# Performance work log

Measured on AMD Instinct MI355X. Metric: run time of the kernel, lower is better.

Reference implementation:

```python
import jax, jax.numpy as jnp
import numpy as np

# Dims: B batch, C=P channels (features per pixel), H*W=N pixels, M ELM models, Q=1 hidden units
M, Q, B, C, H, W_SP = 4, 1, 32, 1024, 28, 28
P = C
N = H * W_SP
EPS = 1e-10


def _lcg_weights(m, n, seed):
    """Deterministic LCG pseudo-random weights, z-score standardized (ELM_AE init)."""
    L = m * n
    a, b, c = L + 2, L + 3, float(L) ** 2
    v = np.zeros(L, dtype=np.float64)
    v[0] = seed + 1.0
    for i in range(1, L):
        v[i] = (a * v[i - 1] + b) % c
    v = (v - v.mean()) / (v.std() + EPS)
    return v.reshape(m, n).astype(np.float32)


def setup_inputs() -> dict:
    key = jax.random.key(0)
    x = jax.random.normal(key, (B, C, H, W_SP), dtype=jnp.float32)
    # One Q x P random input-weight matrix per ELM model, seed = model * (Q * P)
    Wm = jnp.stack([jnp.asarray(_lcg_weights(Q, P, model * (Q * P))) for model in range(M)])  # [M, Q, P]
    return {"x": x, "Wm": Wm}


def reference(x, Wm):
    b, c, h, w = x.shape
    # _norm('l2', ...): per-channel L2 normalization over (h, w), as F.normalize(dim=(1,2))
    norms = jnp.linalg.norm(x.reshape(b, c, h * w), axis=-1)[:, :, None, None]  # [B, C, 1, 1]
    xn = x / jnp.maximum(norms, EPS)
    X = xn.reshape(b, c, h * w)  # meta activation map per sample: [B, P, N]
    # ELM-AE hidden layer, batched over (sample, model): g = sigmoid(W @ X)
    G = jax.nn.sigmoid(jnp.einsum('mqp,bpn->bmqn', Wm, X))  # [B, M, Q, N]
    # fit_AE: output weights beta = pinv(g^T) @ X^T  -> [Q, P]
    pinvGt = jnp.linalg.pinv(jnp.swapaxes(G, -1, -2))       # [B, M, Q, N]
    beta = jnp.einsum('bmqn,bpn->bmqp', pinvGt, X)          # [B, M, Q, P]
    # sum over the M models; Q == 1 so flatten (Q, P) -> Q*P features
    feats = beta.sum(axis=1).reshape(b, -1)                 # [B, Q*P]
    return jnp.nan_to_num(feats)
```

## Files before the change

### kernel.cpp

```cpp
#include <hip/hip_runtime.h>
#include <math.h>

#define BATCH 32
#define CH    1024
#define NPix  784
#define MMOD  4
#define NPC   64
#define PPC   16
#define K1B   256
#define NF4   196
#define T2    832

__device__ __forceinline__ float wave_reduce(float s) {
    #pragma unroll
    for (int off = 32; off; off >>= 1) s += __shfl_down(s, off, 64);
    return s;
}

__device__ __forceinline__ float dpp_wave_sum(float v) {
    int x;
    x = __builtin_amdgcn_update_dpp(0, __builtin_bit_cast(int, v), 0x111, 0xf, 0xf, true);
    v += __builtin_bit_cast(float, x);
    x = __builtin_amdgcn_update_dpp(0, __builtin_bit_cast(int, v), 0x112, 0xf, 0xf, true);
    v += __builtin_bit_cast(float, x);
    x = __builtin_amdgcn_update_dpp(0, __builtin_bit_cast(int, v), 0x114, 0xf, 0xf, true);
    v += __builtin_bit_cast(float, x);
    x = __builtin_amdgcn_update_dpp(0, __builtin_bit_cast(int, v), 0x118, 0xf, 0xf, true);
    v += __builtin_bit_cast(float, x);
    x = __builtin_amdgcn_update_dpp(0, __builtin_bit_cast(int, v), 0x142, 0xa, 0xf, true);
    v += __builtin_bit_cast(float, x);
    x = __builtin_amdgcn_update_dpp(0, __builtin_bit_cast(int, v), 0x143, 0xc, 0xf, true);
    v += __builtin_bit_cast(float, x);
    return v;
}

__global__ __launch_bounds__(K1B) void k_nz(const float* __restrict__ x,
                                            const float* __restrict__ Wm,
                                            float* __restrict__ inv_norm,
                                            float* __restrict__ zpart) {
    __shared__ float sq_l[PPC][4];
    __shared__ float4 wl4[PPC];
    const int blk = blockIdx.x;
    const int b  = blk >> 6;
    const int pc = blk & (NPC - 1);
    const int t = threadIdx.x;
    const int wv = t >> 6, lane = t & 63;
    const bool act = (t < NF4);
    const float4* xb4 = (const float4*)(x + ((size_t)b * CH + (size_t)pc * PPC) * NPix);
    const int tt = act ? t : 0;

    float4 xv[PPC];
    #pragma unroll
    for (int pp = 0; pp < PPC; pp++) xv[pp] = xb4[pp * NF4 + tt];

    #pragma unroll
    for (int pp = 0; pp < PPC; pp++) {
        float4 v = xv[pp];
        float s = act ? (v.x*v.x + v.y*v.y + v.z*v.z + v.w*v.w) : 0.f;
        s = dpp_wave_sum(s);
        if (lane == 63) sq_l[pp][wv] = s;
    }
    __syncthreads();

    if (t < PPC) {
        const float s = sq_l[t][0] + sq_l[t][1] + sq_l[t][2] + sq_l[t][3];
        const float inv = 1.f / fmaxf(sqrtf(s), 1e-10f);
        const int p = pc * PPC + t;
        inv_norm[b * CH + p] = inv;
        float4 w4;
        w4.x = Wm[0 * CH + p] * inv;
        w4.y = Wm[1 * CH + p] * inv;
        w4.z = Wm[2 * CH + p] * inv;
        w4.w = Wm[3 * CH + p] * inv;
        wl4[t] = w4;
    }
    __syncthreads();

    if (act) {
        float4 a0 = {0,0,0,0}, a1 = {0,0,0,0}, a2 = {0,0,0,0}, a3 = {0,0,0,0};
        #pragma unroll
        for (int pp = 0; pp < PPC; pp++) {
            const float4 w = wl4[pp];
            const float4 v = xv[pp];
            a0.x += w.x*v.x; a0.y += w.x*v.y; a0.z += w.x*v.z; a0.w += w.x*v.w;
            a1.x += w.y*v.x; a1.y += w.y*v.y; a1.z += w.y*v.z; a1.w += w.y*v.w;
            a2.x += w.z*v.x; a2.y += w.z*v.y; a2.z += w.z*v.z; a2.w += w.z*v.w;
            a3.x += w.w*v.x; a3.y += w.w*v.y; a3.z += w.w*v.z; a3.w += w.w*v.w;
        }
        float4* zp = (float4*)(zpart + ((size_t)blk * MMOD) * NPix);
        zp[0 * NF4 + t] = a0;
        zp[1 * NF4 + t] = a1;
        zp[2 * NF4 + t] = a2;
        zp[3 * NF4 + t] = a3;
    }
}

__global__ __launch_bounds__(T2) void k_gh(const float* __restrict__ zpart,
                                           float* __restrict__ g_out,
                                           float* __restrict__ s2g) {
    __shared__ float red[13];
    const int blk = blockIdx.x;
    const int b = blk >> 2;
    const int m = blk & 3;
    const int t = threadIdx.x;
    const int wv = t >> 6, lane = t & 63;
    const bool act = (t < NPix);

    float z = 0.f;
    if (act) {
        #pragma unroll 8
        for (int pc = 0; pc < NPC; pc++)
            z += zpart[(((size_t)(b * NPC + pc)) * MMOD + m) * NPix + t];
    }
    const float g = act ? 1.f / (1.f + expf(-z)) : 0.f;
    float s = wave_reduce(g * g);
    if (lane == 0) red[wv] = s;
    __syncthreads();
    if (t == 0) {
        float ss = 0.f;
        #pragma unroll
        for (int w = 0; w < 13; w++) ss += red[w];
        s2g[blk] = fmaxf(ss, 1e-30f);
    }
    if (act) g_out[(size_t)blk * NPix + t] = g;
}

__global__ __launch_bounds__(T2) void k_h(const float* __restrict__ g_out,
                                          const float* __restrict__ s2g,
                                          float* __restrict__ h) {
    const int b = blockIdx.x;
    const int t = threadIdx.x;
    if (t < NPix) {
        float hv = 0.f;
        #pragma unroll
        for (int m = 0; m < MMOD; m++)
            hv += g_out[(size_t)(b * MMOD + m) * NPix + t] / s2g[b * MMOD + m];
        h[(size_t)b * NPix + t] = hv;
    }
}

__global__ __launch_bounds__(256) void k_out(const float* __restrict__ x,
                                             const float* __restrict__ h,
                                             const float* __restrict__ inv_norm,
                                             float* __restrict__ out) {
    const int r = blockIdx.x * 4 + (threadIdx.x >> 6);
    const int lane = threadIdx.x & 63;
    const int b = r >> 10;
    const float4* x4 = (const float4*)(x + (size_t)r * NPix);
    const float4* h4 = (const float4*)(h + (size_t)b * NPix);
    float s = 0.f;
    #pragma unroll
    for (int i = 0; i < 3; i++) {
        float4 xv = x4[i * 64 + lane];
        float4 hv = h4[i * 64 + lane];
        s += xv.x*hv.x + xv.y*hv.y + xv.z*hv.z + xv.w*hv.w;
    }
    if (lane < 4) {
        float4 xv = x4[192 + lane];
        float4 hv = h4[192 + lane];
        s += xv.x*hv.x + xv.y*hv.y + xv.z*hv.z + xv.w*hv.w;
    }
    s = wave_reduce(s);
    if (lane == 0) {
        float v = s * inv_norm[r];
        if (!(v == v)) v = 0.f;
        v = fminf(fmaxf(v, -3.402823466e+38f), 3.402823466e+38f);
        out[r] = v;
    }
}

extern "C" void kernel_launch(void* const* d_in, const int* in_sizes, int n_in,
                              void* d_out, int out_size, void* d_ws, size_t ws_size,
                              hipStream_t stream) {
    const float* x  = (const float*)d_in[0];
    const float* Wm = (const float*)d_in[1];
    float* out = (float*)d_out;
    float* wsf = (float*)d_ws;

    float* inv_norm = wsf;
    float* zpart    = inv_norm + BATCH * CH;
    float* g_out    = zpart + (size_t)BATCH * NPC * MMOD * NPix;
    float* s2g      = g_out + (size_t)BATCH * MMOD * NPix;
    float* h        = s2g + BATCH * MMOD;

    k_nz<<<BATCH * NPC, K1B, 0, stream>>>(x, Wm, inv_norm, zpart);
    k_gh<<<BATCH * MMOD, T2, 0, stream>>>(zpart, g_out, s2g);
    k_h<<<BATCH, T2, 0, stream>>>(g_out, s2g, h);
    k_out<<<BATCH * CH / 4, 256, 0, stream>>>(x, h, inv_norm, out);
}
```

Before: 176.1 us.

## Fuse g and h kernels, halve z partials, store partials in fp16

k_nz now processes 32 channels per block using two 256-thread groups that combine their results through shared memory. This halves the number of partial z rows, and the partials are stored as fp16 to cut workspace traffic. The k_gh and k_h kernels are merged into one per-batch kernel that computes the sigmoid, the per-model squared norm and h together, removing a launch and the g_out round trip. The fp16 partials add rounding error to z before the sigmoid, which may affect accuracy.

```diff
diff --git a/kernel.cpp b/kernel.cpp
--- a/kernel.cpp
+++ b/kernel.cpp
@@ -5,11 +5,13 @@
 #define CH    1024
 #define NPix  784
 #define MMOD  4
-#define NPC   64
-#define PPC   16
-#define K1B   256
+#define NPC   32
+#define PPC   32
+#define GCH   16
 #define NF4   196
-#define T2    832
+#define K1B   512
+
+typedef __attribute__((ext_vector_type(4))) _Float16 half4;
 
 __device__ __forceinline__ float wave_reduce(float s) {
     #pragma unroll
@@ -37,28 +39,33 @@
 __global__ __launch_bounds__(K1B) void k_nz(const float* __restrict__ x,
                                             const float* __restrict__ Wm,
                                             float* __restrict__ inv_norm,
-                                            float* __restrict__ zpart) {
+                                            half4* __restrict__ zpart) {
     __shared__ float sq_l[PPC][4];
     __shared__ float4 wl4[PPC];
+    __shared__ float4 zl[NF4][MMOD];
     const int blk = blockIdx.x;
-    const int b  = blk >> 6;
+    const int b  = blk >> 5;
     const int pc = blk & (NPC - 1);
     const int t = threadIdx.x;
-    const int wv = t >> 6, lane = t & 63;
-    const bool act = (t < NF4);
+    const int g = t >> 8;
+    const int lt = t & 255;
+    const int gwv = (t >> 6) & 3;
+    const int lane = t & 63;
+    const bool act = lt < NF4;
     const float4* xb4 = (const float4*)(x + ((size_t)b * CH + (size_t)pc * PPC) * NPix);
-    const int tt = act ? t : 0;
-
-    float4 xv[PPC];
-    #pragma unroll
-    for (int pp = 0; pp < PPC; pp++) xv[pp] = xb4[pp * NF4 + tt];
-
-    #pragma unroll
-    for (int pp = 0; pp < PPC; pp++) {
+    const int tt = act ? lt : 0;
+
+    float4 xv[GCH];
+    #pragma unroll
+    for (int pp = 0; pp < GCH; pp++)
+        xv[pp] = xb4[(g * GCH + pp) * NF4 + tt];
+
+    #pragma unroll
+    for (int pp = 0; pp < GCH; pp++) {
         float4 v = xv[pp];
         float s = act ? (v.x*v.x + v.y*v.y + v.z*v.z + v.w*v.w) : 0.f;
         s = dpp_wave_sum(s);
-        if (lane == 63) sq_l[pp][wv] = s;
+        if (lane == 63) sq_l[g * GCH + pp][gwv] = s;
     }
     __syncthreads();
 
@@ -76,66 +83,84 @@
     }
     __syncthreads();
 
+    float4 a0 = {0,0,0,0}, a1 = {0,0,0,0}, a2 = {0,0,0,0}, a3 = {0,0,0,0};
     if (act) {
-        float4 a0 = {0,0,0,0}, a1 = {0,0,0,0}, a2 = {0,0,0,0}, a3 = {0,0,0,0};
         #pragma unroll
-        for (int pp = 0; pp < PPC; pp++) {
-            const float4 w = wl4[pp];
+        for (int pp = 0; pp < GCH; pp++) {
+            const float4 w = wl4[g * GCH + pp];
             const float4 v = xv[pp];
             a0.x += w.x*v.x; a0.y += w.x*v.y; a0.z += w.x*v.z; a0.w += w.x*v.w;
             a1.x += w.y*v.x; a1.y += w.y*v.y; a1.z += w.y*v.z; a1.w += w.y*v.w;
             a2.x += w.z*v.x; a2.y += w.z*v.y; a2.z += w.z*v.z; a2.w += w.z*v.w;
             a3.x += w.w*v.x; a3.y += w.w*v.y; a3.z += w.w*v.z; a3.w += w.w*v.w;
         }
-        float4* zp = (float4*)(zpart + ((size_t)blk * MMOD) * NPix);
-        zp[0 * NF4 + t] = a0;
-        zp[1 * NF4 + t] = a1;
-        zp[2 * NF4 + t] = a2;
-        zp[3 * NF4 + t] = a3;
-    }
-}
-
-__global__ __launch_bounds__(T2) void k_gh(const float* __restrict__ zpart,
-                                           float* __restrict__ g_out,
-                                           float* __restrict__ s2g) {
-    __shared__ float red[13];
-    const int blk = blockIdx.x;
-    const int b = blk >> 2;
-    const int m = blk & 3;
+        if (g == 1) {
+            zl[lt][0] = a0; zl[lt][1] = a1; zl[lt][2] = a2; zl[lt][3] = a3;
+        }
+    }
+    __syncthreads();
+    if (g == 0 && act) {
+        float4 b0 = zl[lt][0], b1 = zl[lt][1], b2 = zl[lt][2], b3 = zl[lt][3];
+        a0.x += b0.x; a0.y += b0.y; a0.z += b0.z; a0.w += b0.w;
+        a1.x += b1.x; a1.y += b1.y; a1.z += b1.z; a1.w += b1.w;
+        a2.x += b2.x; a2.y += b2.y; a2.z += b2.z; a2.w += b2.w;
+        a3.x += b3.x; a3.y += b3.y; a3.z += b3.z; a3.w += b3.w;
+        half4* zp = zpart + ((size_t)blk * MMOD) * NF4;
+        half4 h0 = { (_Float16)a0.x, (_Float16)a0.y, (_Float16)a0.z, (_Float16)a0.w };
+        half4 h1 = { (_Float16)a1.x, (_Float16)a1.y, (_Float16)a1.z, (_Float16)a1.w };
+        half4 h2 = { (_Float16)a2.x, (_Float16)a2.y, (_Float16)a2.z, (_Float16)a2.w };
+        half4 h3 = { (_Float16)a3.x, (_Float16)a3.y, (_Float16)a3.z, (_Float16)a3.w };
+        zp[0 * NF4 + lt] = h0;
+        zp[1 * NF4 + lt] = h1;
+        zp[2 * NF4 + lt] = h2;
+        zp[3 * NF4 + lt] = h3;
+    }
+}
+
+__global__ __launch_bounds__(256) void k_gh(const half4* __restrict__ zpart,
+                                            float* __restrict__ h) {
+    __shared__ float red[4][MMOD];
+    __shared__ float s2s[MMOD];
+    const int b = blockIdx.x;
     const int t = threadIdx.x;
     const int wv = t >> 6, lane = t & 63;
-    const bool act = (t < NPix);
-
-    float z = 0.f;
+    const bool act = t < NF4;
+    const int tt = act ? t : 0;
+
+    float4 g4[MMOD];
+    #pragma unroll
+    for (int m = 0; m < MMOD; m++) {
+        float4 z = {0,0,0,0};
+        #pragma unroll 8
+        for (int pc = 0; pc < NPC; pc++) {
+            half4 v = zpart[(((size_t)(b * NPC + pc)) * MMOD + m) * NF4 + tt];
+            z.x += (float)v.x; z.y += (float)v.y; z.z += (float)v.z; z.w += (float)v.w;
+        }
+        float4 gg;
+        gg.x = 1.f / (1.f + expf(-z.x));
+        gg.y = 1.f / (1.f + expf(-z.y));
+        gg.z = 1.f / (1.f + expf(-z.z));
+        gg.w = 1.f / (1.f + expf(-z.w));
+        if (!act) gg = (float4){0,0,0,0};
+        g4[m] = gg;
+        float s = dpp_wave_sum(gg.x*gg.x + gg.y*gg.y + gg.z*gg.z + gg.w*gg.w);
+        if (lane == 63) red[wv][m] = s;
+    }
+    __syncthreads();
+    if (t < MMOD) {
+        float s = red[0][t] + red[1][t] + red[2][t] + red[3][t];
+        s2s[t] = fmaxf(s, 1e-30f);
+    }
+    __syncthreads();
     if (act) {
-        #pragma unroll 8
-        for (int pc = 0; pc < NPC; pc++)
-            z += zpart[(((size_t)(b * NPC + pc)) * MMOD + m) * NPix + t];
-    }
-    const float g = act ? 1.f / (1.f + expf(-z)) : 0.f;
-    float s = wave_reduce(g * g);
-    if (lane == 0) red[wv] = s;
-    __syncthreads();
-    if (t == 0) {
-        float ss = 0.f;
+        float4 hv = {0,0,0,0};
         #pragma unroll
-        for (int w = 0; w < 13; w++) ss += red[w];
-        s2g[blk] = fmaxf(ss, 1e-30f);
-    }
-    if (act) g_out[(size_t)blk * NPix + t] = g;
-}
-
-__global__ __launch_bounds__(T2) void k_h(const float* __restrict__ g_out,
-                                          const float* __restrict__ s2g,
-                                          float* __restrict__ h) {
-    const int b = blockIdx.x;
-    const int t = threadIdx.x;
-    if (t < NPix) {
-        float hv = 0.f;
-        #pragma unroll
-        for (int m = 0; m < MMOD; m++)
-            hv += g_out[(size_t)(b * MMOD + m) * NPix + t] / s2g[b * MMOD + m];
-        h[(size_t)b * NPix + t] = hv;
+        for (int m = 0; m < MMOD; m++) {
+            const float r = 1.f / s2s[m];
+            hv.x += g4[m].x * r; hv.y += g4[m].y * r;
+            hv.z += g4[m].z * r; hv.w += g4[m].w * r;
+        }
+        ((float4*)(h + (size_t)b * NPix))[t] = hv;
     }
 }
 
@@ -178,13 +203,10 @@
     float* wsf = (float*)d_ws;
 
     float* inv_norm = wsf;
-    float* zpart    = inv_norm + BATCH * CH;
-    float* g_out    = zpart + (size_t)BATCH * NPC * MMOD * NPix;
-    float* s2g      = g_out + (size_t)BATCH * MMOD * NPix;
-    float* h        = s2g + BATCH * MMOD;
+    float* h        = inv_norm + BATCH * CH;
+    half4* zpart    = (half4*)(h + BATCH * NPix);
 
     k_nz<<<BATCH * NPC, K1B, 0, stream>>>(x, Wm, inv_norm, zpart);
-    k_gh<<<BATCH * MMOD, T2, 0, stream>>>(zpart, g_out, s2g);
-    k_h<<<BATCH, T2, 0, stream>>>(g_out, s2g, h);
+    k_gh<<<BATCH, 256, 0, stream>>>(zpart, h);
     k_out<<<BATCH * CH / 4, 256, 0, stream>>>(x, h, inv_norm, out);
 }
```

Result: no change. 177.5 us (+0.8%).
